# Optimization experiments

Measured on AMD Instinct MI355X. Metric: run time of the kernel, lower is better.

## Reference

```python
import jax, jax.numpy as jnp
import numpy as np
import math

B, C, N, M = 4, 128, 4096, 4096

def setup_inputs() -> dict:
    key = jax.random.key(0)
    ks = jax.random.split(key, 8)
    return {
        "x1": jax.random.normal(ks[0], (B, C, N), dtype=jnp.float32),
        "p1": jax.random.normal(ks[1], (B, 3, N), dtype=jnp.float32),
        "x2": jax.random.normal(ks[2], (B, C, M), dtype=jnp.float32),
        "p2": jax.random.normal(ks[3], (B, 3, M), dtype=jnp.float32),
        "Wq": jax.random.normal(ks[4], (C, C), dtype=jnp.float32) * 0.05,
        "Wk": jax.random.normal(ks[5], (C, C), dtype=jnp.float32) * 0.05,
        "Wv": jax.random.normal(ks[6], (C, C), dtype=jnp.float32) * 0.05,
        "Wpos": jax.random.normal(ks[7], (C, 3), dtype=jnp.float32) * 0.05,
    }

def reference(x1, p1, x2, p2, Wq, Wk, Wv, Wpos):
    # Conv1d with kernel_size=1, no bias == per-point matmul over channel dim.
    # NOTE: original forward uses self.pos for BOTH p1 and p2 (pos1 conv unused).
    pos = jnp.einsum('ck,bkn->bcn', Wpos, p1)   # [B,C,N]
    pos1 = jnp.einsum('ck,bkm->bcm', Wpos, p2)  # [B,C,M]
    q = jnp.einsum('dc,bcn->bdn', Wq, x1 + pos)   # [B,C,N]
    k = jnp.einsum('dc,bcm->bdm', Wk, x2 + pos1)  # [B,C,M]
    v = jnp.einsum('dc,bcm->bdm', Wv, x2)         # [B,C,M]
    scale = math.sqrt(q.shape[1])  # sqrt(C) -- q.shape[-2] in (B,C,N) layout
    energy = jnp.einsum('bcn,bcm->bnm', q, k) / scale  # [B,N,M]
    attention = jax.nn.softmax(energy, axis=-1)
    vout = jnp.einsum('bnm,bcm->bnc', attention, v)    # [B,N,C]
    out = jnp.swapaxes(vout, 1, 2) + x1                # [B,C,N] residual
    return jnp.swapaxes(out, 1, 2)                     # [B,N,C]
```

## Files before the change

### kernel.cpp

```cpp
#include <hip/hip_runtime.h>
#include <hip/hip_bf16.h>

#define B_ 4
#define C_ 128
#define N_ 4096
#define M_ 4096

typedef __bf16 bf16;
typedef __bf16 bf16x8 __attribute__((ext_vector_type(8)));
typedef float f32x4 __attribute__((ext_vector_type(4)));
typedef float f32x16 __attribute__((ext_vector_type(16)));

#define MFMA16(a, b, c) __builtin_amdgcn_mfma_f32_16x16x32_bf16(a, b, c, 0, 0, 0)
#define MFMA32(a, b, c) __builtin_amdgcn_mfma_f32_32x32x16_bf16(a, b, c, 0, 0, 0)

__device__ inline void gll16(const bf16* g, bf16* l) {
    __builtin_amdgcn_global_load_lds(
        (const __attribute__((address_space(1))) void*)g,
        (__attribute__((address_space(3))) void*)l, 16, 0, 0);
}

__device__ inline unsigned cvtpk(float a, float b) {
    unsigned r;
    asm("v_cvt_pk_bf16_f32 %0, %1, %2" : "=v"(r) : "v"(a), "v"(b));
    return r;
}

__global__ __launch_bounds__(256) void wcvt_kernel(
    const float* __restrict__ Wq, const float* __restrict__ Wk,
    const float* __restrict__ Wv, bf16* __restrict__ Wb) {
    int i = (blockIdx.x * 256 + threadIdx.x) * 4;
    const float* src = (i < 16384) ? Wq : (i < 32768) ? Wk : Wv;
    int off = i & 16383;
    float4 v = *(const float4*)(src + off);
    union { ushort4 u4; bf16 h[4]; } pk;
    pk.h[0] = (bf16)v.x; pk.h[1] = (bf16)v.y;
    pk.h[2] = (bf16)v.z; pk.h[3] = (bf16)v.w;
    *(ushort4*)(Wb + i) = pk.u4;
}

__global__ __launch_bounds__(768) void proj_kernel(
    const float* __restrict__ x1, const float* __restrict__ p1,
    const float* __restrict__ x2, const float* __restrict__ p2,
    const bf16* __restrict__ Wb, const float* __restrict__ Wpos,
    bf16* __restrict__ Qt, bf16* __restrict__ Kt, bf16* __restrict__ Vt) {
    __shared__ __align__(16) bf16 xp1[64 * 136];
    __shared__ __align__(16) bf16 xp2[64 * 136];
    __shared__ __align__(16) bf16 xr2[64 * 136];
    __shared__ float pp1[3 * 64], pp2[3 * 64], wls[384];

    const int t = threadIdx.x;
    const int b = blockIdx.y;
    const int n0 = blockIdx.x * 64;

    if (t < 48) {
        int k3 = t / 16, i4 = (t & 15) * 4;
        *(float4*)&pp1[k3 * 64 + i4] = *(const float4*)(p1 + ((size_t)b * 3 + k3) * N_ + n0 + i4);
    } else if (t < 96) {
        int tt = t - 48;
        int k3 = tt / 16, i4 = (tt & 15) * 4;
        *(float4*)&pp2[k3 * 64 + i4] = *(const float4*)(p2 + ((size_t)b * 3 + k3) * N_ + n0 + i4);
    } else if (t < 192) {
        int i4 = (t - 96) * 4;
        *(float4*)&wls[i4] = *(const float4*)(Wpos + i4);
    }
    __syncthreads();

    for (int s = t; s < 2048; s += 768) {
        int c = s >> 4, n4 = (s & 15) * 4;
        float4 xv = *(const float4*)(x1 + ((size_t)b * C_ + c) * N_ + n0 + n4);
        float w0 = wls[c * 3 + 0], w1 = wls[c * 3 + 1], w2 = wls[c * 3 + 2];
        const float* xa = &xv.x;
        #pragma unroll
        for (int j = 0; j < 4; ++j) {
            float pos = w0 * pp1[n4 + j] + w1 * pp1[64 + n4 + j] + w2 * pp1[128 + n4 + j];
            xp1[(n4 + j) * 136 + c] = (bf16)(xa[j] + pos);
        }
    }
    for (int s = t; s < 2048; s += 768) {
        int c = s >> 4, n4 = (s & 15) * 4;
        float4 xv = *(const float4*)(x2 + ((size_t)b * C_ + c) * N_ + n0 + n4);
        float w0 = wls[c * 3 + 0], w1 = wls[c * 3 + 1], w2 = wls[c * 3 + 2];
        const float* xa = &xv.x;
        #pragma unroll
        for (int j = 0; j < 4; ++j) {
            float pos = w0 * pp2[n4 + j] + w1 * pp2[64 + n4 + j] + w2 * pp2[128 + n4 + j];
            xp2[(n4 + j) * 136 + c] = (bf16)(xa[j] + pos);
            xr2[(n4 + j) * 136 + c] = (bf16)xa[j];
        }
    }
    __syncthreads();

    const int w = t >> 6;
    const int lane = t & 63;
    const int col = lane & 15, quad = lane >> 4;
    const int role = w >> 2, band = w & 3;
    const int nl = band * 16 + col;
    const int n = n0 + nl;

    const bf16* src = (role == 0) ? xp1 : (role == 1) ? xp2 : xr2;
    const bf16* Wm = Wb + role * 16384;

    bf16x8 bx[4];
    #pragma unroll
    for (int cs = 0; cs < 4; ++cs)
        bx[cs] = *(const bf16x8*)&src[nl * 136 + cs * 32 + quad * 8];

    #pragma unroll
    for (int dt = 0; dt < 8; ++dt) {
        f32x4 acc = {0.f, 0.f, 0.f, 0.f};
        #pragma unroll
        for (int cs = 0; cs < 4; ++cs) {
            bf16x8 wf = *(const bf16x8*)(Wm + (dt * 16 + col) * 128 + cs * 32 + quad * 8);
            acc = MFMA16(wf, bx[cs], acc);
        }
        if (role < 2) {
            bf16* Ot = (role == 0) ? Qt : Kt;
            union { ushort4 u4; bf16 h[4]; } pk;
            #pragma unroll
            for (int r = 0; r < 4; ++r) pk.h[r] = (bf16)acc[r];
            *(ushort4*)(Ot + ((size_t)b * N_ + n) * C_ + dt * 16 + quad * 4) = pk.u4;
        } else {
            #pragma unroll
            for (int r = 0; r < 4; ++r)
                Vt[((size_t)b * C_ + dt * 16 + quad * 4 + r) * (size_t)M_ + n] = (bf16)acc[r];
        }
    }
}

__global__ __launch_bounds__(256, 2) void attn_kernel(
    const bf16* __restrict__ Qt, const bf16* __restrict__ Kt,
    const bf16* __restrict__ Vt, const float* __restrict__ x1,
    float* __restrict__ out) {
    __shared__ __align__(16) char smem[66048];
    bf16* kb = (bf16*)smem;
    bf16* vb = (bf16*)(smem + 32768);

    const int t = threadIdx.x;
    const int w = t >> 6;
    const int lane = t & 63;
    const int col = lane & 31;
    const int hi = lane >> 5;

    const int g0 = blockIdx.x;
    const int xcd = g0 & 7;
    const int b = xcd >> 1;
    const int qt = (xcd & 1) + ((g0 >> 3) << 1);
    const int n0 = qt * 32;

    const float KS = 0.12752107168406815f;

    const bf16* Kbase = Kt + (size_t)b * M_ * C_;
    const bf16* Vbase = Vt + (size_t)b * C_ * M_;

    bf16x8 qf[8];
    {
        const bf16* Qb = Qt + ((size_t)b * N_ + n0 + col) * C_ + hi * 8;
        #pragma unroll
        for (int cs = 0; cs < 8; ++cs)
            qf[cs] = *(const bf16x8*)(Qb + cs * 16);
    }

    f32x16 oacc[4];
    #pragma unroll
    for (int i = 0; i < 4; ++i)
        #pragma unroll
        for (int j = 0; j < 16; ++j) oacc[i][j] = 0.f;
    float lacc = 0.f;

    const int key_l = (w << 5) + col;
    const char* kbp = (const char*)kb + key_l * 256;
    const int kxor = (key_l & 15) << 4;

    auto stageK = [&](int m0) {
        #pragma unroll
        for (int i = 0; i < 8; ++i) {
            int g = ((w << 3) + i) * 64 + lane;
            int key = g >> 4;
            int sp = (g & 15) ^ (key & 15);
            gll16(Kbase + (size_t)(m0 + key) * C_ + sp * 8, kb + ((w << 3) + i) * 512);
        }
    };
    auto stageV = [&](int m0) {
        #pragma unroll
        for (int i = 0; i < 8; ++i) {
            int g = ((w << 3) + i) * 64 + lane;
            int c = g >> 4;
            int sp = (g & 15) ^ (c & 15);
            gll16(Vbase + (size_t)c * M_ + m0 + sp * 8, vb + ((w << 3) + i) * 512);
        }
    };

    stageK(0);
    stageV(0);

    for (int ch = 0; ch < 32; ++ch) {
        asm volatile("s_waitcnt vmcnt(8)" ::: "memory");
        __builtin_amdgcn_sched_barrier(0);

        f32x16 s0a, s1a;
        #pragma unroll
        for (int j = 0; j < 16; ++j) { s0a[j] = 0.f; s1a[j] = 0.f; }
        __builtin_amdgcn_s_setprio(1);
        #pragma unroll
        for (int cs = 0; cs < 4; ++cs) {
            bf16x8 kf = *(const bf16x8*)(kbp + ((((cs << 1) + hi) << 4) ^ kxor));
            s0a = MFMA32(kf, qf[cs], s0a);
        }
        #pragma unroll
        for (int cs = 4; cs < 8; ++cs) {
            bf16x8 kf = *(const bf16x8*)(kbp + ((((cs << 1) + hi) << 4) ^ kxor));
            s1a = MFMA32(kf, qf[cs], s1a);
        }
        __builtin_amdgcn_s_setprio(0);

        if (ch < 31) {
            asm volatile("s_waitcnt lgkmcnt(0)" ::: "memory");
            __builtin_amdgcn_sched_barrier(0);
            stageK((ch + 1) << 7);
        }

        float p[16];
        #pragma unroll
        for (int r = 0; r < 16; ++r) {
            float e = fminf((s0a[r] + s1a[r]) * KS, 60.f);
            p[r] = __builtin_amdgcn_exp2f(e);
        }
        {
            float s01 = (p[0] + p[1]) + (p[2] + p[3]);
            float s23 = (p[4] + p[5]) + (p[6] + p[7]);
            float s45 = (p[8] + p[9]) + (p[10] + p[11]);
            float s67 = (p[12] + p[13]) + (p[14] + p[15]);
            lacc += (s01 + s23) + (s45 + s67);
        }
        unsigned W0 = cvtpk(p[0], p[1]),  W1 = cvtpk(p[2], p[3]);
        unsigned W2 = cvtpk(p[4], p[5]),  W3 = cvtpk(p[6], p[7]);
        unsigned W4 = cvtpk(p[8], p[9]),  W5 = cvtpk(p[10], p[11]);
        unsigned W6 = cvtpk(p[12], p[13]), W7 = cvtpk(p[14], p[15]);
        unsigned X0 = hi ? W0 : W2, X1 = hi ? W1 : W3;
        unsigned Y0 = hi ? W4 : W6, Y1 = hi ? W5 : W7;
        X0 = __shfl_xor(X0, 32, 64);  X1 = __shfl_xor(X1, 32, 64);
        Y0 = __shfl_xor(Y0, 32, 64);  Y1 = __shfl_xor(Y1, 32, 64);
        uint4 u0, u1;
        u0.x = hi ? X0 : W0;  u0.y = hi ? X1 : W1;
        u0.z = hi ? W2 : X0;  u0.w = hi ? W3 : X1;
        u1.x = hi ? Y0 : W4;  u1.y = hi ? Y1 : W5;
        u1.z = hi ? W6 : Y0;  u1.w = hi ? W7 : Y1;
        bf16x8 af0 = __builtin_bit_cast(bf16x8, u0);
        bf16x8 af1 = __builtin_bit_cast(bf16x8, u1);

        if (ch < 31) asm volatile("s_waitcnt vmcnt(8)" ::: "memory");
        else         asm volatile("s_waitcnt vmcnt(0)" ::: "memory");
        __builtin_amdgcn_sched_barrier(0);
        __builtin_amdgcn_s_barrier();

        __builtin_amdgcn_s_setprio(1);
        #pragma unroll
        for (int ct = 0; ct < 4; ++ct) {
            int c = (ct << 5) + col;
            const char* vbp = (const char*)vb + c * 256;
            int vxor = (c & 15) << 4;
            bf16x8 vf0 = *(const bf16x8*)(vbp + ((((w << 2) + hi) << 4) ^ vxor));
            bf16x8 vf1 = *(const bf16x8*)(vbp + ((((w << 2) + 2 + hi) << 4) ^ vxor));
            oacc[ct] = MFMA32(af0, vf0, oacc[ct]);
            oacc[ct] = MFMA32(af1, vf1, oacc[ct]);
        }
        __builtin_amdgcn_s_setprio(0);

        asm volatile("s_waitcnt lgkmcnt(0)" ::: "memory");
        __builtin_amdgcn_sched_barrier(0);
        __builtin_amdgcn_s_barrier();
        if (ch < 31) stageV((ch + 1) << 7);
    }

    __builtin_amdgcn_s_barrier();

    float* obuf = (float*)smem;
    float* lps  = (float*)(smem + 65536);

    lacc += __shfl_xor(lacc, 32, 64);
    if (hi == 0) lps[(w << 5) + col] = lacc;

    #pragma unroll
    for (int ct = 0; ct < 4; ++ct)
        #pragma unroll
        for (int r = 0; r < 16; ++r) {
            int q = (r & 3) + ((r >> 2) << 3) + (hi << 2);
            obuf[w * 4096 + q * 128 + (ct << 5) + col] = oacc[ct][r];
        }
    __syncthreads();

    const int c2 = lane << 1;
    #pragma unroll
    for (int j = 0; j < 8; ++j) {
        int q = (w << 3) + j;
        float s0 = 0.f, s1 = 0.f;
        #pragma unroll
        for (int pp = 0; pp < 4; ++pp) {
            float2 v = *(const float2*)&obuf[pp * 4096 + q * 128 + c2];
            s0 += v.x; s1 += v.y;
        }
        float lsum = lps[q] + lps[32 + q] + lps[64 + q] + lps[96 + q];
        float linv = 1.0f / lsum;
        int n = n0 + q;
        float o0 = s0 * linv + x1[((size_t)b * C_ + c2) * N_ + n];
        float o1 = s1 * linv + x1[((size_t)b * C_ + c2 + 1) * N_ + n];
        *(float2*)&out[((size_t)b * N_ + n) * C_ + c2] = make_float2(o0, o1);
    }
}

extern "C" void kernel_launch(void* const* d_in, const int* in_sizes, int n_in,
                              void* d_out, int out_size, void* d_ws, size_t ws_size,
                              hipStream_t stream) {
    const float* x1   = (const float*)d_in[0];
    const float* p1   = (const float*)d_in[1];
    const float* x2   = (const float*)d_in[2];
    const float* p2   = (const float*)d_in[3];
    const float* Wq   = (const float*)d_in[4];
    const float* Wk   = (const float*)d_in[5];
    const float* Wv   = (const float*)d_in[6];
    const float* Wpos = (const float*)d_in[7];
    float* out = (float*)d_out;

    bf16* Qt = (bf16*)d_ws;
    bf16* Kt = Qt + (size_t)B_ * N_ * C_;
    bf16* Vt = Kt + (size_t)B_ * M_ * C_;

    bf16* Wb = (bf16*)d_out;

    wcvt_kernel<<<dim3(48), dim3(256), 0, stream>>>(Wq, Wk, Wv, Wb);
    proj_kernel<<<dim3(64, B_), dim3(768), 0, stream>>>(
        x1, p1, x2, p2, Wb, Wpos, Qt, Kt, Vt);
    attn_kernel<<<dim3(512), dim3(256), 0, stream>>>(Qt, Kt, Vt, x1, out);
}
```

Baseline: 152.8 us.

## Share double-buffered K/V tiles across 64 queries per block; coalesce V stores

The attention kernel now runs 512-thread blocks. Two query groups of 32 rows share each staged K/V chunk, and K/V are double-buffered in 132 KB of LDS so the next chunk loads while the current one is computed, with one barrier per iteration. This halves K/V global/L2 traffic per query and simplifies the wait/barrier schedule. In exchange, only one block fits per CU and the grid drops to 256 blocks. The projection kernel also transposes V through LDS so V is written with coalesced 16-byte stores instead of strided 2-byte ones.

```diff
diff --git a/kernel.cpp b/kernel.cpp
--- a/kernel.cpp
+++ b/kernel.cpp
@@ -44,9 +44,10 @@
     const float* __restrict__ x2, const float* __restrict__ p2,
     const bf16* __restrict__ Wb, const float* __restrict__ Wpos,
     bf16* __restrict__ Qt, bf16* __restrict__ Kt, bf16* __restrict__ Vt) {
-    __shared__ __align__(16) bf16 xp1[64 * 136];
-    __shared__ __align__(16) bf16 xp2[64 * 136];
-    __shared__ __align__(16) bf16 xr2[64 * 136];
+    __shared__ __align__(16) bf16 xbuf[3 * 64 * 136];
+    bf16* xp1 = xbuf;
+    bf16* xp2 = xbuf + 8704;
+    bf16* xr2 = xbuf + 17408;
     __shared__ float pp1[3 * 64], pp2[3 * 64], wls[384];
 
     const int t = threadIdx.x;
@@ -106,6 +107,9 @@
     for (int cs = 0; cs < 4; ++cs)
         bx[cs] = *(const bf16x8*)&src[nl * 136 + cs * 32 + quad * 8];
 
+    __syncthreads();
+    bf16* vt = xbuf;
+
     #pragma unroll
     for (int dt = 0; dt < 8; ++dt) {
         f32x4 acc = {0.f, 0.f, 0.f, 0.f};
@@ -123,30 +127,37 @@
         } else {
             #pragma unroll
             for (int r = 0; r < 4; ++r)
-                Vt[((size_t)b * C_ + dt * 16 + quad * 4 + r) * (size_t)M_ + n] = (bf16)acc[r];
-        }
-    }
-}
-
-__global__ __launch_bounds__(256, 2) void attn_kernel(
+                vt[(dt * 16 + quad * 4 + r) * 72 + nl] = (bf16)acc[r];
+        }
+    }
+    __syncthreads();
+
+    for (int s = t; s < 1024; s += 768) {
+        int c = s >> 3, off = s & 7;
+        *(uint4*)(Vt + ((size_t)b * C_ + c) * (size_t)M_ + n0 + off * 8) =
+            *(const uint4*)&vt[c * 72 + off * 8];
+    }
+}
+
+__global__ __launch_bounds__(512) void attn_kernel(
     const bf16* __restrict__ Qt, const bf16* __restrict__ Kt,
     const bf16* __restrict__ Vt, const float* __restrict__ x1,
     float* __restrict__ out) {
-    __shared__ __align__(16) char smem[66048];
-    bf16* kb = (bf16*)smem;
-    bf16* vb = (bf16*)(smem + 32768);
+    __shared__ __align__(16) char smem[132096];
 
     const int t = threadIdx.x;
     const int w = t >> 6;
     const int lane = t & 63;
     const int col = lane & 31;
     const int hi = lane >> 5;
+    const int kg = w & 3;
+    const int qg = w >> 2;
 
     const int g0 = blockIdx.x;
     const int xcd = g0 & 7;
     const int b = xcd >> 1;
     const int qt = (xcd & 1) + ((g0 >> 3) << 1);
-    const int n0 = qt * 32;
+    const int n0 = qt * 64;
 
     const float KS = 0.12752107168406815f;
 
@@ -155,7 +166,7 @@
 
     bf16x8 qf[8];
     {
-        const bf16* Qb = Qt + ((size_t)b * N_ + n0 + col) * C_ + hi * 8;
+        const bf16* Qb = Qt + ((size_t)b * N_ + n0 + qg * 32 + col) * C_ + hi * 8;
         #pragma unroll
         for (int cs = 0; cs < 8; ++cs)
             qf[cs] = *(const bf16x8*)(Qb + cs * 16);
@@ -168,35 +179,45 @@
         for (int j = 0; j < 16; ++j) oacc[i][j] = 0.f;
     float lacc = 0.f;
 
-    const int key_l = (w << 5) + col;
-    const char* kbp = (const char*)kb + key_l * 256;
+    const int key_l = (kg << 5) + col;
     const int kxor = (key_l & 15) << 4;
 
-    auto stageK = [&](int m0) {
-        #pragma unroll
-        for (int i = 0; i < 8; ++i) {
-            int g = ((w << 3) + i) * 64 + lane;
+    auto stageK = [&](int m0, char* dst) {
+        #pragma unroll
+        for (int i = 0; i < 4; ++i) {
+            int g = ((w << 2) + i) * 64 + lane;
             int key = g >> 4;
             int sp = (g & 15) ^ (key & 15);
-            gll16(Kbase + (size_t)(m0 + key) * C_ + sp * 8, kb + ((w << 3) + i) * 512);
+            gll16(Kbase + (size_t)(m0 + key) * C_ + sp * 8,
+                  (bf16*)dst + ((w << 2) + i) * 512);
         }
     };
-    auto stageV = [&](int m0) {
-        #pragma unroll
-        for (int i = 0; i < 8; ++i) {
-            int g = ((w << 3) + i) * 64 + lane;
+    auto stageV = [&](int m0, char* dst) {
+        #pragma unroll
+        for (int i = 0; i < 4; ++i) {
+            int g = ((w << 2) + i) * 64 + lane;
             int c = g >> 4;
             int sp = (g & 15) ^ (c & 15);
-            gll16(Vbase + (size_t)c * M_ + m0 + sp * 8, vb + ((w << 3) + i) * 512);
+            gll16(Vbase + (size_t)c * M_ + m0 + sp * 8,
+                  (bf16*)dst + ((w << 2) + i) * 512);
         }
     };
 
-    stageK(0);
-    stageV(0);
-
+    stageK(0, smem);
+    stageV(0, smem + 65536);
+
+    int buf = 0;
     for (int ch = 0; ch < 32; ++ch) {
-        asm volatile("s_waitcnt vmcnt(8)" ::: "memory");
+        asm volatile("s_waitcnt vmcnt(0)" ::: "memory");
         __builtin_amdgcn_sched_barrier(0);
+        __builtin_amdgcn_s_barrier();
+
+        if (ch < 31) {
+            stageK((ch + 1) << 7, smem + ((buf ^ 1) << 15));
+            stageV((ch + 1) << 7, smem + 65536 + ((buf ^ 1) << 15));
+        }
+
+        const char* kbp = smem + (buf << 15) + key_l * 256;
 
         f32x16 s0a, s1a;
         #pragma unroll
@@ -213,12 +234,6 @@
             s1a = MFMA32(kf, qf[cs], s1a);
         }
         __builtin_amdgcn_s_setprio(0);
-
-        if (ch < 31) {
-            asm volatile("s_waitcnt lgkmcnt(0)" ::: "memory");
-            __builtin_amdgcn_sched_barrier(0);
-            stageK((ch + 1) << 7);
-        }
 
         float p[16];
         #pragma unroll
@@ -249,19 +264,15 @@
         bf16x8 af0 = __builtin_bit_cast(bf16x8, u0);
         bf16x8 af1 = __builtin_bit_cast(bf16x8, u1);
 
-        if (ch < 31) asm volatile("s_waitcnt vmcnt(8)" ::: "memory");
-        else         asm volatile("s_waitcnt vmcnt(0)" ::: "memory");
-        __builtin_amdgcn_sched_barrier(0);
-        __builtin_amdgcn_s_barrier();
-
+        const char* vbB = smem + 65536 + (buf << 15);
         __builtin_amdgcn_s_setprio(1);
         #pragma unroll
         for (int ct = 0; ct < 4; ++ct) {
             int c = (ct << 5) + col;
-            const char* vbp = (const char*)vb + c * 256;
+            const char* vbp = vbB + c * 256;
             int vxor = (c & 15) << 4;
-            bf16x8 vf0 = *(const bf16x8*)(vbp + ((((w << 2) + hi) << 4) ^ vxor));
-            bf16x8 vf1 = *(const bf16x8*)(vbp + ((((w << 2) + 2 + hi) << 4) ^ vxor));
+            bf16x8 vf0 = *(const bf16x8*)(vbp + ((((kg << 2) + hi) << 4) ^ vxor));
+            bf16x8 vf1 = *(const bf16x8*)(vbp + ((((kg << 2) + 2 + hi) << 4) ^ vxor));
             oacc[ct] = MFMA32(af0, vf0, oacc[ct]);
             oacc[ct] = MFMA32(af1, vf1, oacc[ct]);
         }
@@ -269,24 +280,23 @@
 
         asm volatile("s_waitcnt lgkmcnt(0)" ::: "memory");
         __builtin_amdgcn_sched_barrier(0);
-        __builtin_amdgcn_s_barrier();
-        if (ch < 31) stageV((ch + 1) << 7);
+        buf ^= 1;
     }
 
     __builtin_amdgcn_s_barrier();
 
     float* obuf = (float*)smem;
-    float* lps  = (float*)(smem + 65536);
+    float* lps  = (float*)(smem + 131072);
 
     lacc += __shfl_xor(lacc, 32, 64);
-    if (hi == 0) lps[(w << 5) + col] = lacc;
+    if (hi == 0) lps[(kg << 6) + (qg << 5) + col] = lacc;
 
     #pragma unroll
     for (int ct = 0; ct < 4; ++ct)
         #pragma unroll
         for (int r = 0; r < 16; ++r) {
             int q = (r & 3) + ((r >> 2) << 3) + (hi << 2);
-            obuf[w * 4096 + q * 128 + (ct << 5) + col] = oacc[ct][r];
+            obuf[kg * 8192 + ((qg << 5) + q) * 128 + (ct << 5) + col] = oacc[ct][r];
         }
     __syncthreads();
 
@@ -297,10 +307,10 @@
         float s0 = 0.f, s1 = 0.f;
         #pragma unroll
         for (int pp = 0; pp < 4; ++pp) {
-            float2 v = *(const float2*)&obuf[pp * 4096 + q * 128 + c2];
+            float2 v = *(const float2*)&obuf[pp * 8192 + q * 128 + c2];
             s0 += v.x; s1 += v.y;
         }
-        float lsum = lps[q] + lps[32 + q] + lps[64 + q] + lps[96 + q];
+        float lsum = lps[q] + lps[64 + q] + lps[128 + q] + lps[192 + q];
         float linv = 1.0f / lsum;
         int n = n0 + q;
         float o0 = s0 * linv + x1[((size_t)b * C_ + c2) * N_ + n];
@@ -331,5 +341,5 @@
     wcvt_kernel<<<dim3(48), dim3(256), 0, stream>>>(Wq, Wk, Wv, Wb);
     proj_kernel<<<dim3(64, B_), dim3(768), 0, stream>>>(
         x1, p1, x2, p2, Wb, Wpos, Qt, Kt, Vt);
-    attn_kernel<<<dim3(512), dim3(256), 0, stream>>>(Qt, Kt, Vt, x1, out);
-}
+    attn_kernel<<<dim3(256), dim3(512), 0, stream>>>(Qt, Kt, Vt, x1, out);
+}
```

Result: faster. 146.3 us (-4.2%).
